# Optimization experiments

Hardware: AMD Instinct MI355X
Metric: run time of the kernel (lower is better)

The kernel has to match this reference:

```python
import jax, jax.numpy as jnp
import numpy as np

TEMPERATURE = 0.07
EPS = 1e-8  # torch F.cosine_similarity eps


def reference(features):
    B, F, D = features.shape
    x = features.reshape(B * F, D)  # [N, D]
    # cosine similarity = normalized-dot; torch clamps norm at eps
    norm = jnp.maximum(jnp.linalg.norm(x, axis=-1, keepdims=True), EPS)
    xn = x / norm
    logits = (xn @ xn.T) / TEMPERATURE  # [N, N]
    # cross_entropy with labels = arange(N): mean(logsumexp - diagonal)
    lse = jax.scipy.special.logsumexp(logits, axis=-1)
    diag = jnp.diagonal(logits)
    return jnp.mean(lse - diag)


def setup_inputs() -> dict:
    key = jax.random.key(0)
    features = jax.random.normal(key, (512, 16, 512), dtype=jnp.float32)
    return {"features": features}
```

## Files before the change

### kernel.cpp

```cpp
#include <hip/hip_runtime.h>
#include <hip/hip_bf16.h>
#include <cstdint>

#define N_TOT 8192
#define DDIM  512
#define DBYTES 512
#define NBLK  64
#define NTRI  (NBLK * (NBLK + 1) / 2)
constexpr float INV_T = 1.0f / 0.07f;

typedef uint8_t u8;
typedef __attribute__((ext_vector_type(8))) int i32x8_t;
typedef __attribute__((ext_vector_type(4))) float f32x4_t;


__device__ __forceinline__ void load16_to_lds(const void* g, void* l) {
  __builtin_amdgcn_global_load_lds(
      (const __attribute__((address_space(1))) unsigned int*)g,
      (__attribute__((address_space(3))) unsigned int*)l, 16, 0, 0);
}

__global__ __launch_bounds__(256) void normalize_kernel(const float* __restrict__ X,
                                                        u8* __restrict__ Xn,
                                                        float* __restrict__ tsum,
                                                        float* __restrict__ out) {
  if (blockIdx.x < 32) tsum[blockIdx.x * 256 + threadIdx.x] = 0.0f;
  if (blockIdx.x == 32 && threadIdx.x == 0) out[0] = 0.0f;
  const int lane = threadIdx.x & 63;
  const int row  = blockIdx.x * 4 + (threadIdx.x >> 6);
  const float4* xr = (const float4*)(X + (size_t)row * DDIM);
  float4 v0 = xr[lane];
  float4 v1 = xr[lane + 64];
  float s = v0.x * v0.x + v0.y * v0.y + v0.z * v0.z + v0.w * v0.w
          + v1.x * v1.x + v1.y * v1.y + v1.z * v1.z + v1.w * v1.w;
#pragma unroll
  for (int m = 1; m < 64; m <<= 1) s += __shfl_xor(s, m);
  const float scale = 1.0f / fmaxf(sqrtf(s), 1e-8f);
  int w0 = __builtin_amdgcn_cvt_pk_fp8_f32(v0.x * scale, v0.y * scale, 0, 0);
  w0     = __builtin_amdgcn_cvt_pk_fp8_f32(v0.z * scale, v0.w * scale, w0, 1);
  int w1 = __builtin_amdgcn_cvt_pk_fp8_f32(v1.x * scale, v1.y * scale, 0, 0);
  w1     = __builtin_amdgcn_cvt_pk_fp8_f32(v1.z * scale, v1.w * scale, w1, 1);
  uint32_t* orow = (uint32_t*)(Xn + (size_t)row * DBYTES);
  orow[lane]      = (uint32_t)w0;
  orow[lane + 64] = (uint32_t)w1;
}

__global__ __launch_bounds__(256, 3) void gemm_exp_rowsum(const u8* __restrict__ Xn,
                                                          float* __restrict__ tsum) {
  __shared__ __align__(16) u8 sA[128 * 128];
  __shared__ __align__(16) u8 sB[128 * 128];

  const int k = blockIdx.x;
  int bi = (int)((sqrtf(8.0f * (float)k + 1.0f) - 1.0f) * 0.5f);
  while ((bi + 1) * (bi + 2) / 2 <= k) ++bi;
  while (bi * (bi + 1) / 2 > k) --bi;
  const int bj = k - bi * (bi + 1) / 2;
  const int rowBase = bi * 128;
  const int colBase = bj * 128;
  const bool isDiag = (bi == bj);

  const int t    = threadIdx.x;
  const int lane = t & 63;
  const int l15  = lane & 15;
  const int quad = lane >> 4;
  const int w    = t >> 6;
  const int wm   = w >> 1;
  const int wn   = w & 1;

  f32x4_t acc[4][4];
#pragma unroll
  for (int i = 0; i < 4; i++)
#pragma unroll
    for (int j = 0; j < 4; j++) acc[i][j] = {0.f, 0.f, 0.f, 0.f};

  const int srow = t >> 3;
  const int goff = ((t & 7) ^ (srow & 7)) * 16;
  const u8* gA = Xn + (size_t)(rowBase + srow) * DBYTES + goff;
  const u8* gB = Xn + (size_t)(colBase + srow) * DBYTES + goff;
  u8* lA = sA + t * 16;
  u8* lB = sB + t * 16;

  for (int k0 = 0; k0 < DBYTES; k0 += 128) {
#pragma unroll
    for (int r = 0; r < 4; r++) {
      load16_to_lds(gA + (size_t)(r * 32) * DBYTES + k0, lA + r * 4096);
      load16_to_lds(gB + (size_t)(r * 32) * DBYTES + k0, lB + r * 4096);
    }
    __syncthreads();

    i32x8_t a[4], b[4];
#pragma unroll
    for (int mi = 0; mi < 4; mi++) {
      const int row = wm * 64 + mi * 16 + l15;
      const int s0 = ((quad * 2) ^ (row & 7)) * 16;
      const int s1 = ((quad * 2 + 1) ^ (row & 7)) * 16;
      int4 lo = *(const int4*)&sA[row * 128 + s0];
      int4 hi = *(const int4*)&sA[row * 128 + s1];
      a[mi] = (i32x8_t){lo.x, lo.y, lo.z, lo.w, hi.x, hi.y, hi.z, hi.w};
    }
#pragma unroll
    for (int ni = 0; ni < 4; ni++) {
      const int row = wn * 64 + ni * 16 + l15;
      const int s0 = ((quad * 2) ^ (row & 7)) * 16;
      const int s1 = ((quad * 2 + 1) ^ (row & 7)) * 16;
      int4 lo = *(const int4*)&sB[row * 128 + s0];
      int4 hi = *(const int4*)&sB[row * 128 + s1];
      b[ni] = (i32x8_t){lo.x, lo.y, lo.z, lo.w, hi.x, hi.y, hi.z, hi.w};
    }

#pragma unroll
    for (int mi = 0; mi < 4; mi++)
#pragma unroll
      for (int ni = 0; ni < 4; ni++)
        acc[mi][ni] = __builtin_amdgcn_mfma_scale_f32_16x16x128_f8f6f4(
            a[mi], b[ni], acc[mi][ni], 0, 0, 0, 0x7F7F7F7Fu, 0, 0x7F7F7F7Fu);
    __syncthreads();
  }

  if (isDiag) {
#pragma unroll
    for (int mi = 0; mi < 4; mi++) {
#pragma unroll
      for (int r = 0; r < 4; r++) {
        const int row = rowBase + wm * 64 + mi * 16 + quad * 4 + r;
        float rs = 0.0f;
#pragma unroll
        for (int ni = 0; ni < 4; ni++) {
          const int col = colBase + wn * 64 + ni * 16 + l15;
          const float e = __expf((acc[mi][ni][r] - 1.0f) * INV_T);
          rs += (row == col) ? 0.0f : e;
        }
        rs += __shfl_xor(rs, 1);
        rs += __shfl_xor(rs, 2);
        rs += __shfl_xor(rs, 4);
        rs += __shfl_xor(rs, 8);
        if (l15 == 0) atomicAdd(&tsum[row], rs);
      }
    }
  } else {
    float csum[4] = {0.f, 0.f, 0.f, 0.f};
#pragma unroll
    for (int mi = 0; mi < 4; mi++) {
#pragma unroll
      for (int r = 0; r < 4; r++) {
        const int row = rowBase + wm * 64 + mi * 16 + quad * 4 + r;
        float rs = 0.0f;
#pragma unroll
        for (int ni = 0; ni < 4; ni++) {
          const float e = __expf((acc[mi][ni][r] - 1.0f) * INV_T);
          rs += e;
          csum[ni] += e;
        }
        rs += __shfl_xor(rs, 1);
        rs += __shfl_xor(rs, 2);
        rs += __shfl_xor(rs, 4);
        rs += __shfl_xor(rs, 8);
        if (l15 == 0) atomicAdd(&tsum[row], rs);
      }
    }
#pragma unroll
    for (int ni = 0; ni < 4; ni++) {
      csum[ni] += __shfl_xor(csum[ni], 16);
      csum[ni] += __shfl_xor(csum[ni], 32);
      if (quad == 0) atomicAdd(&tsum[colBase + wn * 64 + ni * 16 + l15], csum[ni]);
    }
  }
}

__global__ __launch_bounds__(256) void finalize_kernel(const float* __restrict__ tsum,
                                                       float* __restrict__ out) {
  const int i = blockIdx.x * 256 + threadIdx.x;
  float s = log1pf(tsum[i]);
#pragma unroll
  for (int m = 1; m < 64; m <<= 1) s += __shfl_xor(s, m);
  __shared__ float ws[4];
  if ((threadIdx.x & 63) == 0) ws[threadIdx.x >> 6] = s;
  __syncthreads();
  if (threadIdx.x == 0)
    atomicAdd(out, (ws[0] + ws[1] + ws[2] + ws[3]) * (1.0f / N_TOT));
}

extern "C" void kernel_launch(void* const* d_in, const int* in_sizes, int n_in,
                              void* d_out, int out_size, void* d_ws, size_t ws_size,
                              hipStream_t stream) {
  const float* X = (const float*)d_in[0];
  float* out = (float*)d_out;

  float* tsum = (float*)d_ws;
  u8* Xn = (u8*)d_ws + 65536;

  normalize_kernel<<<N_TOT / 4, 256, 0, stream>>>(X, Xn, tsum, out);
  gemm_exp_rowsum<<<NTRI, 256, 0, stream>>>(Xn, tsum);
  finalize_kernel<<<N_TOT / 256, 256, 0, stream>>>(tsum, out);
}
```

Before: 116.0 us.

## Keep full A row-block in LDS and stream up to four B tiles per block

Each block now loads the whole 128x512 fp8 A row-block into LDS once and loops over up to four column tiles of the lower triangle, reading B fragments directly from global memory into registers with a one-step software prefetch. The grid shrinks from 2080 triangular tiles to 544 chunks, and the per-k-step LDS staging and barriers for B are gone. This is meant to cut redundant A loads and synchronisation. In exchange the block uses 64KB of LDS (occupancy bound lowered to 2), B reads are uncoalesced global loads, and chunk work is uneven near the diagonal.

Result: slower. 151.9 us (+31.0%).

```diff
diff --git a/kernel.cpp b/kernel.cpp
--- a/kernel.cpp
+++ b/kernel.cpp
@@ -6,7 +6,7 @@
 #define DDIM  512
 #define DBYTES 512
 #define NBLK  64
-#define NTRI  (NBLK * (NBLK + 1) / 2)
+#define NCHUNK 544
 constexpr float INV_T = 1.0f / 0.07f;
 
 typedef uint8_t u8;
@@ -18,6 +18,19 @@
   __builtin_amdgcn_global_load_lds(
       (const __attribute__((address_space(1))) unsigned int*)g,
       (__attribute__((address_space(3))) unsigned int*)l, 16, 0, 0);
+}
+
+__device__ __forceinline__ void loadB(const u8* __restrict__ Xn, int colBase,
+                                      int wn, int l15, int quad, int kk,
+                                      i32x8_t b[4]) {
+#pragma unroll
+  for (int ni = 0; ni < 4; ni++) {
+    const u8* p = Xn + (size_t)(colBase + wn * 64 + ni * 16 + l15) * DBYTES +
+                  kk * 128 + quad * 32;
+    int4 lo = *(const int4*)p;
+    int4 hi = *(const int4*)(p + 16);
+    b[ni] = (i32x8_t){lo.x, lo.y, lo.z, lo.w, hi.x, hi.y, hi.z, hi.w};
+  }
 }
 
 __global__ __launch_bounds__(256) void normalize_kernel(const float* __restrict__ X,
@@ -45,19 +58,19 @@
   orow[lane + 64] = (uint32_t)w1;
 }
 
-__global__ __launch_bounds__(256, 3) void gemm_exp_rowsum(const u8* __restrict__ Xn,
+__global__ __launch_bounds__(256, 2) void gemm_exp_rowsum(const u8* __restrict__ Xn,
                                                           float* __restrict__ tsum) {
-  __shared__ __align__(16) u8 sA[128 * 128];
-  __shared__ __align__(16) u8 sB[128 * 128];
-
-  const int k = blockIdx.x;
-  int bi = (int)((sqrtf(8.0f * (float)k + 1.0f) - 1.0f) * 0.5f);
-  while ((bi + 1) * (bi + 2) / 2 <= k) ++bi;
-  while (bi * (bi + 1) / 2 > k) --bi;
-  const int bj = k - bi * (bi + 1) / 2;
+  __shared__ __align__(16) u8 sA[128 * 512];
+
+  const int id = blockIdx.x;
+  int g = (int)((sqrtf(1.0f + 2.0f * (float)id) - 1.0f) * 0.5f);
+  while (2 * (g + 1) * (g + 2) <= id) ++g;
+  while (2 * g * (g + 1) > id) --g;
+  const int rem = id - 2 * g * (g + 1);
+  const int bi  = 4 * g + rem / (g + 1);
+  const int c0  = (rem % (g + 1)) * 4;
+  const int ntiles = min(4, bi - c0 + 1);
   const int rowBase = bi * 128;
-  const int colBase = bj * 128;
-  const bool isDiag = (bi == bj);
 
   const int t    = threadIdx.x;
   const int lane = t & 63;
@@ -67,102 +80,107 @@
   const int wm   = w >> 1;
   const int wn   = w & 1;
 
-  f32x4_t acc[4][4];
-#pragma unroll
-  for (int i = 0; i < 4; i++)
-#pragma unroll
-    for (int j = 0; j < 4; j++) acc[i][j] = {0.f, 0.f, 0.f, 0.f};
-
-  const int srow = t >> 3;
-  const int goff = ((t & 7) ^ (srow & 7)) * 16;
-  const u8* gA = Xn + (size_t)(rowBase + srow) * DBYTES + goff;
-  const u8* gB = Xn + (size_t)(colBase + srow) * DBYTES + goff;
-  u8* lA = sA + t * 16;
-  u8* lB = sB + t * 16;
-
-  for (int k0 = 0; k0 < DBYTES; k0 += 128) {
-#pragma unroll
-    for (int r = 0; r < 4; r++) {
-      load16_to_lds(gA + (size_t)(r * 32) * DBYTES + k0, lA + r * 4096);
-      load16_to_lds(gB + (size_t)(r * 32) * DBYTES + k0, lB + r * 4096);
+  {
+    const int arow = t >> 5;
+    const int akk  = (t >> 3) & 3;
+    const int ajl  = (t & 7) ^ (arow & 7);
+    const u8* gsrc = Xn + (size_t)(rowBase + arow) * DBYTES + akk * 128 + ajl * 16;
+    u8* ldst = sA + t * 16;
+#pragma unroll
+    for (int i = 0; i < 16; i++)
+      load16_to_lds(gsrc + (size_t)i * 4096, ldst + i * 4096);
+  }
+
+  i32x8_t bcur[4], bnxt[4];
+  loadB(Xn, c0 * 128, wn, l15, quad, 0, bcur);
+  __syncthreads();
+
+  for (int ti = 0; ti < ntiles; ++ti) {
+    const int colBase = (c0 + ti) * 128;
+    const bool isDiag = (c0 + ti == bi);
+
+    f32x4_t acc[4][4];
+#pragma unroll
+    for (int i = 0; i < 4; i++)
+#pragma unroll
+      for (int j = 0; j < 4; j++) acc[i][j] = {0.f, 0.f, 0.f, 0.f};
+
+#pragma unroll
+    for (int kk = 0; kk < 4; kk++) {
+      if (kk < 3) {
+        loadB(Xn, colBase, wn, l15, quad, kk + 1, bnxt);
+      } else {
+        const int nb = (ti + 1 < ntiles) ? colBase + 128 : colBase;
+        loadB(Xn, nb, wn, l15, quad, 0, bnxt);
+      }
+      i32x8_t a[4];
+#pragma unroll
+      for (int mi = 0; mi < 4; mi++) {
+        const int row = wm * 64 + mi * 16 + l15;
+        const int base = row * 512 + kk * 128;
+        const int s0 = (((quad * 2) ^ (row & 7)) * 16);
+        const int s1 = (((quad * 2 + 1) ^ (row & 7)) * 16);
+        int4 lo = *(const int4*)&sA[base + s0];
+        int4 hi = *(const int4*)&sA[base + s1];
+        a[mi] = (i32x8_t){lo.x, lo.y, lo.z, lo.w, hi.x, hi.y, hi.z, hi.w};
+      }
+#pragma unroll
+      for (int mi = 0; mi < 4; mi++)
+#pragma unroll
+        for (int ni = 0; ni < 4; ni++)
+          acc[mi][ni] = __builtin_amdgcn_mfma_scale_f32_16x16x128_f8f6f4(
+              a[mi], bcur[ni], acc[mi][ni], 0, 0, 0, 0x7F7F7F7Fu, 0, 0x7F7F7F7Fu);
+#pragma unroll
+      for (int ni = 0; ni < 4; ni++) bcur[ni] = bnxt[ni];
     }
-    __syncthreads();
-
-    i32x8_t a[4], b[4];
-#pragma unroll
-    for (int mi = 0; mi < 4; mi++) {
-      const int row = wm * 64 + mi * 16 + l15;
-      const int s0 = ((quad * 2) ^ (row & 7)) * 16;
-      const int s1 = ((quad * 2 + 1) ^ (row & 7)) * 16;
-      int4 lo = *(const int4*)&sA[row * 128 + s0];
-      int4 hi = *(const int4*)&sA[row * 128 + s1];
-      a[mi] = (i32x8_t){lo.x, lo.y, lo.z, lo.w, hi.x, hi.y, hi.z, hi.w};
-    }
-#pragma unroll
-    for (int ni = 0; ni < 4; ni++) {
-      const int row = wn * 64 + ni * 16 + l15;
-      const int s0 = ((quad * 2) ^ (row & 7)) * 16;
-      const int s1 = ((quad * 2 + 1) ^ (row & 7)) * 16;
-      int4 lo = *(const int4*)&sB[row * 128 + s0];
-      int4 hi = *(const int4*)&sB[row * 128 + s1];
-      b[ni] = (i32x8_t){lo.x, lo.y, lo.z, lo.w, hi.x, hi.y, hi.z, hi.w};
-    }
-
-#pragma unroll
-    for (int mi = 0; mi < 4; mi++)
-#pragma unroll
-      for (int ni = 0; ni < 4; ni++)
-        acc[mi][ni] = __builtin_amdgcn_mfma_scale_f32_16x16x128_f8f6f4(
-            a[mi], b[ni], acc[mi][ni], 0, 0, 0, 0x7F7F7F7Fu, 0, 0x7F7F7F7Fu);
-    __syncthreads();
-  }
-
-  if (isDiag) {
-#pragma unroll
-    for (int mi = 0; mi < 4; mi++) {
-#pragma unroll
-      for (int r = 0; r < 4; r++) {
-        const int row = rowBase + wm * 64 + mi * 16 + quad * 4 + r;
-        float rs = 0.0f;
-#pragma unroll
-        for (int ni = 0; ni < 4; ni++) {
-          const int col = colBase + wn * 64 + ni * 16 + l15;
-          const float e = __expf((acc[mi][ni][r] - 1.0f) * INV_T);
-          rs += (row == col) ? 0.0f : e;
+
+    if (isDiag) {
+#pragma unroll
+      for (int mi = 0; mi < 4; mi++) {
+#pragma unroll
+        for (int r = 0; r < 4; r++) {
+          const int row = rowBase + wm * 64 + mi * 16 + quad * 4 + r;
+          float rs = 0.0f;
+#pragma unroll
+          for (int ni = 0; ni < 4; ni++) {
+            const int col = colBase + wn * 64 + ni * 16 + l15;
+            const float e = __expf((acc[mi][ni][r] - 1.0f) * INV_T);
+            rs += (row == col) ? 0.0f : e;
+          }
+          rs += __shfl_xor(rs, 1);
+          rs += __shfl_xor(rs, 2);
+          rs += __shfl_xor(rs, 4);
+          rs += __shfl_xor(rs, 8);
+          if (l15 == 0) atomicAdd(&tsum[row], rs);
         }
-        rs += __shfl_xor(rs, 1);
-        rs += __shfl_xor(rs, 2);
-        rs += __shfl_xor(rs, 4);
-        rs += __shfl_xor(rs, 8);
-        if (l15 == 0) atomicAdd(&tsum[row], rs);
-      }
-    }
-  } else {
-    float csum[4] = {0.f, 0.f, 0.f, 0.f};
-#pragma unroll
-    for (int mi = 0; mi < 4; mi++) {
-#pragma unroll
-      for (int r = 0; r < 4; r++) {
-        const int row = rowBase + wm * 64 + mi * 16 + quad * 4 + r;
-        float rs = 0.0f;
-#pragma unroll
-        for (int ni = 0; ni < 4; ni++) {
-          const float e = __expf((acc[mi][ni][r] - 1.0f) * INV_T);
-          rs += e;
-          csum[ni] += e;
+      }
+    } else {
+      float csum[4] = {0.f, 0.f, 0.f, 0.f};
+#pragma unroll
+      for (int mi = 0; mi < 4; mi++) {
+#pragma unroll
+        for (int r = 0; r < 4; r++) {
+          const int row = rowBase + wm * 64 + mi * 16 + quad * 4 + r;
+          float rs = 0.0f;
+#pragma unroll
+          for (int ni = 0; ni < 4; ni++) {
+            const float e = __expf((acc[mi][ni][r] - 1.0f) * INV_T);
+            rs += e;
+            csum[ni] += e;
+          }
+          rs += __shfl_xor(rs, 1);
+          rs += __shfl_xor(rs, 2);
+          rs += __shfl_xor(rs, 4);
+          rs += __shfl_xor(rs, 8);
+          if (l15 == 0) atomicAdd(&tsum[row], rs);
         }
-        rs += __shfl_xor(rs, 1);
-        rs += __shfl_xor(rs, 2);
-        rs += __shfl_xor(rs, 4);
-        rs += __shfl_xor(rs, 8);
-        if (l15 == 0) atomicAdd(&tsum[row], rs);
-      }
-    }
-#pragma unroll
-    for (int ni = 0; ni < 4; ni++) {
-      csum[ni] += __shfl_xor(csum[ni], 16);
-      csum[ni] += __shfl_xor(csum[ni], 32);
-      if (quad == 0) atomicAdd(&tsum[colBase + wn * 64 + ni * 16 + l15], csum[ni]);
+      }
+#pragma unroll
+      for (int ni = 0; ni < 4; ni++) {
+        csum[ni] += __shfl_xor(csum[ni], 16);
+        csum[ni] += __shfl_xor(csum[ni], 32);
+        if (quad == 0) atomicAdd(&tsum[colBase + wn * 64 + ni * 16 + l15], csum[ni]);
+      }
     }
   }
 }
@@ -190,6 +208,6 @@
   u8* Xn = (u8*)d_ws + 65536;
 
   normalize_kernel<<<N_TOT / 4, 256, 0, stream>>>(X, Xn, tsum, out);
-  gemm_exp_rowsum<<<NTRI, 256, 0, stream>>>(Xn, tsum);
+  gemm_exp_rowsum<<<NCHUNK, 256, 0, stream>>>(Xn, tsum);
   finalize_kernel<<<N_TOT / 256, 256, 0, stream>>>(tsum, out);
 }
```

## Prefetch next K tile into registers during MFMA, replacing direct global-to-LDS loads

Applied to the files above, without the earlier changes.

Replaces the global_load_lds direct-to-LDS copies with register-staged loads. The next K-slice is fetched into registers while the current slice's MFMAs run, then written to LDS between two barriers. This is meant to hide global memory latency behind compute. The cost is extra VGPRs, which may hurt the 3-blocks-per-SM occupancy target, plus an extra barrier per iteration.

After: 162.3 us. 1.4x slower.

```diff
diff --git a/kernel.cpp b/kernel.cpp
--- a/kernel.cpp
+++ b/kernel.cpp
@@ -12,13 +12,6 @@
 typedef uint8_t u8;
 typedef __attribute__((ext_vector_type(8))) int i32x8_t;
 typedef __attribute__((ext_vector_type(4))) float f32x4_t;
-
-
-__device__ __forceinline__ void load16_to_lds(const void* g, void* l) {
-  __builtin_amdgcn_global_load_lds(
-      (const __attribute__((address_space(1))) unsigned int*)g,
-      (__attribute__((address_space(3))) unsigned int*)l, 16, 0, 0);
-}
 
 __global__ __launch_bounds__(256) void normalize_kernel(const float* __restrict__ X,
                                                         u8* __restrict__ Xn,
@@ -80,20 +73,27 @@
   u8* lA = sA + t * 16;
   u8* lB = sB + t * 16;
 
-  for (int k0 = 0; k0 < DBYTES; k0 += 128) {
-#pragma unroll
-    for (int r = 0; r < 4; r++) {
-      load16_to_lds(gA + (size_t)(r * 32) * DBYTES + k0, lA + r * 4096);
-      load16_to_lds(gB + (size_t)(r * 32) * DBYTES + k0, lB + r * 4096);
-    }
-    __syncthreads();
-
+  int4 vA[4], vB[4];
+#pragma unroll
+  for (int r = 0; r < 4; r++) {
+    vA[r] = *(const int4*)(gA + (size_t)(r * 32) * DBYTES);
+    vB[r] = *(const int4*)(gB + (size_t)(r * 32) * DBYTES);
+  }
+#pragma unroll
+  for (int r = 0; r < 4; r++) {
+    *(int4*)(lA + r * 4096) = vA[r];
+    *(int4*)(lB + r * 4096) = vB[r];
+  }
+  __syncthreads();
+
+#pragma unroll
+  for (int it = 0; it < 4; ++it) {
     i32x8_t a[4], b[4];
 #pragma unroll
     for (int mi = 0; mi < 4; mi++) {
       const int row = wm * 64 + mi * 16 + l15;
-      const int s0 = ((quad * 2) ^ (row & 7)) * 16;
-      const int s1 = ((quad * 2 + 1) ^ (row & 7)) * 16;
+      const int s0 = (((quad * 2) ^ (row & 7)) * 16);
+      const int s1 = (((quad * 2 + 1) ^ (row & 7)) * 16);
       int4 lo = *(const int4*)&sA[row * 128 + s0];
       int4 hi = *(const int4*)&sA[row * 128 + s1];
       a[mi] = (i32x8_t){lo.x, lo.y, lo.z, lo.w, hi.x, hi.y, hi.z, hi.w};
@@ -101,20 +101,38 @@
 #pragma unroll
     for (int ni = 0; ni < 4; ni++) {
       const int row = wn * 64 + ni * 16 + l15;
-      const int s0 = ((quad * 2) ^ (row & 7)) * 16;
-      const int s1 = ((quad * 2 + 1) ^ (row & 7)) * 16;
+      const int s0 = (((quad * 2) ^ (row & 7)) * 16);
+      const int s1 = (((quad * 2 + 1) ^ (row & 7)) * 16);
       int4 lo = *(const int4*)&sB[row * 128 + s0];
       int4 hi = *(const int4*)&sB[row * 128 + s1];
       b[ni] = (i32x8_t){lo.x, lo.y, lo.z, lo.w, hi.x, hi.y, hi.z, hi.w};
     }
 
+    if (it < 3) {
+      const int k0 = (it + 1) * 128;
+#pragma unroll
+      for (int r = 0; r < 4; r++) {
+        vA[r] = *(const int4*)(gA + (size_t)(r * 32) * DBYTES + k0);
+        vB[r] = *(const int4*)(gB + (size_t)(r * 32) * DBYTES + k0);
+      }
+    }
+
 #pragma unroll
     for (int mi = 0; mi < 4; mi++)
 #pragma unroll
       for (int ni = 0; ni < 4; ni++)
         acc[mi][ni] = __builtin_amdgcn_mfma_scale_f32_16x16x128_f8f6f4(
             a[mi], b[ni], acc[mi][ni], 0, 0, 0, 0x7F7F7F7Fu, 0, 0x7F7F7F7Fu);
-    __syncthreads();
+
+    if (it < 3) {
+      __syncthreads();
+#pragma unroll
+      for (int r = 0; r < 4; r++) {
+        *(int4*)(lA + r * 4096) = vA[r];
+        *(int4*)(lB + r * 4096) = vB[r];
+      }
+      __syncthreads();
+    }
   }
 
   if (isDiag) {
```
